# Kernel tuning notes

Hardware: AMD Instinct MI355X
Metric: run time of the kernel (lower is better)

## Reference

```python
import jax, jax.numpy as jnp
import numpy as np

NUM_EXPERTS = 8
DIM = 2048
BATCH = 8192


def setup_inputs() -> dict:
    key = jax.random.key(0)
    k_x, k_ids, k_w, k_b = jax.random.split(key, 4)
    x = jax.random.normal(k_x, (BATCH, DIM), dtype=jnp.float32)
    cam_pred_ids = jax.random.randint(k_ids, (BATCH,), 0, NUM_EXPERTS, dtype=jnp.int64)
    # torch nn.Linear default init: U(-1/sqrt(in), 1/sqrt(in)); W is [out, in]
    bound = 1.0 / np.sqrt(DIM)
    W = jax.random.uniform(k_w, (NUM_EXPERTS, DIM, DIM), dtype=jnp.float32,
                           minval=-bound, maxval=bound)
    b = jax.random.uniform(k_b, (NUM_EXPERTS, DIM), dtype=jnp.float32,
                           minval=-bound, maxval=bound)
    return {"x": x, "cam_pred_ids": cam_pred_ids, "W": W, "b": b}


def reference(x, cam_pred_ids, W, b):
    # Per-sample expert routing: out[i] = x[i] + relu(x[i] @ W[e].T + b[e]),
    # where e = cam_pred_ids[i]. Vectorized as 8 full-batch GEMMs with masked
    # combine (fixed small expert count -> Python loop is structural, not data).
    h = jnp.zeros_like(x)
    for e in range(NUM_EXPERTS):
        he = jax.nn.relu(x @ W[e].T + b[e])          # [B, D]
        mask = (cam_pred_ids == e)[:, None]
        h = h + jnp.where(mask, he, jnp.zeros((), dtype=x.dtype))
    return x + h
```

## Files before the change

### kernel.cpp

```cpp
#include <hip/hip_runtime.h>
#include <hip/hip_bf16.h>
#include <stdint.h>

#define BATCH 8192
#define DIM   2048
#define NEXP  8
#define BM    128
#define BN    128
#define BK    32
#define NITER (DIM / BK)
#define MAX_TILES 72
#define NBLK  (DIM / BN)
#define NCVTB 4096

typedef __bf16 bf16x8 __attribute__((ext_vector_type(8)));
typedef float  f32x4  __attribute__((ext_vector_type(4)));

#define WB_BYTE_OFF 37789696ull
#define WS_NEED     104898560ull

#define AS1(p) ((const __attribute__((address_space(1))) void*)(p))
#define AS3(p) ((__attribute__((address_space(3))) void*)(p))

__device__ __forceinline__ unsigned f2bf2(float lo, float hi) {
    unsigned ul = __float_as_uint(lo), uh = __float_as_uint(hi);
    ul = (ul + 0x7FFFu + ((ul >> 16) & 1u)) >> 16;
    uh = (uh + 0x7FFFu + ((uh >> 16) & 1u)) >> 16;
    return (uh << 16) | ul;
}

__global__ __launch_bounds__(512)
void k_prep(const int* __restrict__ ids, int* __restrict__ ws,
            int* __restrict__ rowmap,
            const float4* __restrict__ W, uint4* __restrict__ Wb) {
    int b = blockIdx.x;
    int t = threadIdx.x;
    if (b > 0) {
        size_t base = (size_t)(b - 1) * 1024;
#pragma unroll
        for (int j = 0; j < 2; j++) {
            size_t o = base + (size_t)j * 512 + t;
            float4 a = W[o * 2], c = W[o * 2 + 1];
            uint4 v;
            v.x = f2bf2(a.x, a.y);  v.y = f2bf2(a.z, a.w);
            v.z = f2bf2(c.x, c.y);  v.w = f2bf2(c.z, c.w);
            Wb[o] = v;
        }
        return;
    }
    __shared__ int sc[512 * NEXP];
    __shared__ int seg[NEXP];
    __shared__ int tot[NEXP];
    int myids[16];
    int base = t * 16;
#pragma unroll
    for (int e = 0; e < NEXP; e++) sc[t * NEXP + e] = 0;
#pragma unroll
    for (int i = 0; i < 16; i++) {
        myids[i] = ids[base + i];
        sc[t * NEXP + myids[i]]++;
    }
    __syncthreads();
    {
        int w = t >> 6, l = t & 63;
        int e = w;
        int vals[8], sum = 0;
#pragma unroll
        for (int j = 0; j < 8; j++) { vals[j] = sc[(l * 8 + j) * NEXP + e]; sum += vals[j]; }
        int inc = sum;
        for (int d = 1; d < 64; d <<= 1) {
            int v = __shfl_up(inc, d, 64);
            if (l >= d) inc += v;
        }
        int run = inc - sum;
#pragma unroll
        for (int j = 0; j < 8; j++) { int v = vals[j]; sc[(l * 8 + j) * NEXP + e] = run; run += v; }
        if (l == 63) tot[e] = run;
    }
    __syncthreads();
    if (t == 0) {
        int pos = 0, mt = 0;
        for (int e = 0; e < NEXP; e++) {
            int c = tot[e];
            seg[e] = pos;
            int ntl = (c + BM - 1) / BM;
            for (int tt = 0; tt < ntl; tt++) {
                ws[64  + mt] = e;
                ws[160 + mt] = pos + tt * BM;
                int v = c - tt * BM;
                ws[256 + mt] = v < BM ? v : BM;
                mt++;
            }
            pos += ntl * BM;
        }
        ws[48] = mt;
    }
    __syncthreads();
#pragma unroll
    for (int i = 0; i < 16; i++) {
        int e = myids[i];
        int p = seg[e] + sc[t * NEXP + e]++;
        rowmap[p] = base + i;
    }
}

__launch_bounds__(256)
__global__ void k_gemm(const float* __restrict__ x,
                       const unsigned short* __restrict__ Wb,
                       const float* __restrict__ bias,
                       const int* __restrict__ ws, const int* __restrict__ rowmap,
                       float* __restrict__ out) {
    int nb = blockIdx.x;
    int mt = blockIdx.y;
    if (mt >= ws[48]) return;
    int e     = ws[64  + mt];
    int pos0  = ws[160 + mt];
    int valid = ws[256 + mt];
    int n0 = nb * BN;

    __shared__ unsigned short lds[2][8192];

    int tid = threadIdx.x;
    int w = tid >> 6, l = tid & 63;
    int lane15 = l & 15, quad = l >> 4;
    int wave_m = (w >> 1) * 64, wave_n = (w & 1) * 64;

    const unsigned short* Bbase = Wb + (size_t)e * DIM * DIM + (size_t)n0 * DIM;

    int arow  = w * 32 + (l >> 1);
    int ahalf = l & 1;
    int s_r = (arow >> 1) & 3;
    int aw0 = arow * BK + (((ahalf * 2)    ) ^ s_r) * 8;
    int aw1 = arow * BK + (((ahalf * 2) + 1) ^ s_r) * 8;
    bool aval = arow < valid;
    const float4* asrc = nullptr;
    if (aval)
        asrc = (const float4*)(x + (size_t)rowmap[pos0 + arow] * DIM + ahalf * 16);

    int srcOff[2];
#pragma unroll
    for (int j = 0; j < 2; j++) {
        int c = w * 128 + j * 64 + l;
        int row = c >> 2, pos = c & 3;
        int q = pos ^ ((row >> 1) & 3);
        srcOff[j] = row * DIM + q * 8;
    }

    int swz = (quad ^ ((lane15 >> 1) & 3)) * 8;
    int afOff[4], bfOff[4];
#pragma unroll
    for (int mi = 0; mi < 4; mi++)
        afOff[mi] = (wave_m + mi * 16 + lane15) * BK + swz;
#pragma unroll
    for (int ni = 0; ni < 4; ni++)
        bfOff[ni] = 4096 + (wave_n + ni * 16 + lane15) * BK + swz;

    f32x4 acc[4][4];
#pragma unroll
    for (int i = 0; i < 4; i++)
#pragma unroll
        for (int j = 0; j < 4; j++) acc[i][j] = (f32x4){0.f, 0.f, 0.f, 0.f};

#define ISSUE_B(buf, k0)                                                        \
    do {                                                                        \
        _Pragma("unroll")                                                       \
        for (int j = 0; j < 2; j++) {                                           \
            __builtin_amdgcn_global_load_lds(                                   \
                AS1(Bbase + (k0) + srcOff[j]),                                  \
                AS3(&lds[buf][4096 + w * 1024 + j * 512]), 16, 0, 0);           \
        }                                                                       \
    } while (0)

#define CVT_WRITE(buf, a0, a1, a2, a3)                                          \
    do {                                                                        \
        bf16x8 c0, c1;                                                          \
        c0[0] = (__bf16)a0.x; c0[1] = (__bf16)a0.y;                             \
        c0[2] = (__bf16)a0.z; c0[3] = (__bf16)a0.w;                             \
        c0[4] = (__bf16)a1.x; c0[5] = (__bf16)a1.y;                             \
        c0[6] = (__bf16)a1.z; c0[7] = (__bf16)a1.w;                             \
        c1[0] = (__bf16)a2.x; c1[1] = (__bf16)a2.y;                             \
        c1[2] = (__bf16)a2.z; c1[3] = (__bf16)a2.w;                             \
        c1[4] = (__bf16)a3.x; c1[5] = (__bf16)a3.y;                             \
        c1[6] = (__bf16)a3.z; c1[7] = (__bf16)a3.w;                             \
        *(bf16x8*)(&lds[buf][aw0]) = c0;                                        \
        *(bf16x8*)(&lds[buf][aw1]) = c1;                                        \
    } while (0)

    {
        float4 a0 = {0,0,0,0}, a1 = {0,0,0,0}, a2 = {0,0,0,0}, a3 = {0,0,0,0};
        if (aval) { a0 = asrc[0]; a1 = asrc[1]; a2 = asrc[2]; a3 = asrc[3]; }
        CVT_WRITE(0, a0, a1, a2, a3);
        ISSUE_B(0, 0);
    }
    int cur = 0;
    for (int i = 0; i < NITER; ++i) {
        __syncthreads();
        float4 a0 = {0,0,0,0}, a1 = {0,0,0,0}, a2 = {0,0,0,0}, a3 = {0,0,0,0};
        if (i + 1 < NITER) {
            if (aval) {
                const float4* p = asrc + (i + 1) * (BK / 4);
                a0 = p[0]; a1 = p[1]; a2 = p[2]; a3 = p[3];
            }
            ISSUE_B(cur ^ 1, (i + 1) * BK);
        }
        bf16x8 af[4], bf[4];
#pragma unroll
        for (int mi = 0; mi < 4; mi++)
            af[mi] = *(const bf16x8*)(&lds[cur][afOff[mi]]);
#pragma unroll
        for (int ni = 0; ni < 4; ni++)
            bf[ni] = *(const bf16x8*)(&lds[cur][bfOff[ni]]);
#pragma unroll
        for (int mi = 0; mi < 4; mi++)
#pragma unroll
            for (int ni = 0; ni < 4; ni++)
                acc[mi][ni] = __builtin_amdgcn_mfma_f32_16x16x32_bf16(
                    af[mi], bf[ni], acc[mi][ni], 0, 0, 0);
        if (i + 1 < NITER)
            CVT_WRITE(cur ^ 1, a0, a1, a2, a3);
        cur ^= 1;
    }
#undef ISSUE_B
#undef CVT_WRITE

    float bv[4];
#pragma unroll
    for (int ni = 0; ni < 4; ni++)
        bv[ni] = bias[(size_t)e * DIM + n0 + wave_n + ni * 16 + lane15];
#pragma unroll
    for (int mi = 0; mi < 4; mi++) {
#pragma unroll
        for (int r4 = 0; r4 < 4; r4++) {
            int rl = wave_m + mi * 16 + quad * 4 + r4;
            if (rl < valid) {
                int orig = rowmap[pos0 + rl];
                const float* xrow = x + (size_t)orig * DIM + n0;
                float* orow = out + (size_t)orig * DIM + n0;
#pragma unroll
                for (int ni = 0; ni < 4; ni++) {
                    int col = wave_n + ni * 16 + lane15;
                    float v = acc[mi][ni][r4] + bv[ni];
                    v = v > 0.f ? v : 0.f;
                    orow[col] = xrow[col] + v;
                }
            }
        }
    }
}

__global__ void k_naive(const float* __restrict__ x, const int* __restrict__ ids,
                        const float* __restrict__ W, const float* __restrict__ b,
                        float* __restrict__ out) {
    __shared__ float lx[DIM];
    int i = blockIdx.x;
    for (int t = threadIdx.x; t < DIM; t += blockDim.x) lx[t] = x[(size_t)i * DIM + t];
    __syncthreads();
    int e = ids[i];
    const float* We = W + (size_t)e * DIM * DIM;
    for (int n = threadIdx.x; n < DIM; n += blockDim.x) {
        const float* wr = We + (size_t)n * DIM;
        float acc = 0.f;
        for (int k = 0; k < DIM; k += 4) {
            float4 w4 = *(const float4*)(wr + k);
            acc += lx[k] * w4.x + lx[k + 1] * w4.y + lx[k + 2] * w4.z + lx[k + 3] * w4.w;
        }
        float v = acc + b[(size_t)e * DIM + n];
        v = v > 0.f ? v : 0.f;
        out[(size_t)i * DIM + n] = lx[n] + v;
    }
}

extern "C" void kernel_launch(void* const* d_in, const int* in_sizes, int n_in,
                              void* d_out, int out_size, void* d_ws, size_t ws_size,
                              hipStream_t stream) {
    const float* x   = (const float*)d_in[0];
    const int*   ids = (const int*)d_in[1];
    const float* W   = (const float*)d_in[2];
    const float* b   = (const float*)d_in[3];
    float* out = (float*)d_out;

    if (ws_size < WS_NEED) {
        k_naive<<<BATCH, 256, 0, stream>>>(x, ids, W, b, out);
        return;
    }

    char* wsb = (char*)d_ws;
    int*  wsi = (int*)wsb;
    unsigned short* Wb = (unsigned short*)(wsb + WB_BYTE_OFF);
    int* rowmap = wsi + 512;

    k_prep<<<NCVTB + 1, 512, 0, stream>>>(ids, wsi, rowmap,
                                          (const float4*)W, (uint4*)Wb);
    dim3 g(NBLK, MAX_TILES);
    k_gemm<<<g, 256, 0, stream>>>(x, Wb, b, wsi, rowmap, out);
}
```

Before: 431.6 us.

## Pre-convert x to bf16 and stream A tiles via direct global-to-LDS loads

```diff
diff --git a/kernel.cpp b/kernel.cpp
--- a/kernel.cpp
+++ b/kernel.cpp
@@ -11,11 +11,15 @@
 #define NITER (DIM / BK)
 #define MAX_TILES 72
 #define NBLK  (DIM / BN)
+#define NROWS 9216
+#define NXBB  2048
 #define NCVTB 4096
 
 typedef __bf16 bf16x8 __attribute__((ext_vector_type(8)));
 typedef float  f32x4  __attribute__((ext_vector_type(4)));
 
+#define ZP_BYTE_OFF 40960ull
+#define XB_BYTE_OFF 49152ull
 #define WB_BYTE_OFF 37789696ull
 #define WS_NEED     104898560ull
 
@@ -32,22 +36,27 @@
 __global__ __launch_bounds__(512)
 void k_prep(const int* __restrict__ ids, int* __restrict__ ws,
             int* __restrict__ rowmap,
-            const float4* __restrict__ W, uint4* __restrict__ Wb) {
+            const float4* __restrict__ x4, uint4* __restrict__ xb4,
+            const float4* __restrict__ W, uint4* __restrict__ Wb,
+            int* __restrict__ zp) {
     int b = blockIdx.x;
     int t = threadIdx.x;
     if (b > 0) {
-        size_t base = (size_t)(b - 1) * 1024;
+        const float4* src; uint4* dst; size_t base;
+        if (b <= NXBB) { src = x4; dst = xb4; base = (size_t)(b - 1) * 1024; }
+        else           { src = W;  dst = Wb;  base = (size_t)(b - 1 - NXBB) * 1024; }
 #pragma unroll
         for (int j = 0; j < 2; j++) {
             size_t o = base + (size_t)j * 512 + t;
-            float4 a = W[o * 2], c = W[o * 2 + 1];
+            float4 a = src[o * 2], c = src[o * 2 + 1];
             uint4 v;
             v.x = f2bf2(a.x, a.y);  v.y = f2bf2(a.z, a.w);
             v.z = f2bf2(c.x, c.y);  v.w = f2bf2(c.z, c.w);
-            Wb[o] = v;
+            dst[o] = v;
         }
         return;
     }
+    zp[t] = 0; zp[t + 512] = 0;
     __shared__ int sc[512 * NEXP];
     __shared__ int seg[NEXP];
     __shared__ int tot[NEXP];
@@ -96,6 +105,8 @@
         ws[48] = mt;
     }
     __syncthreads();
+    for (int i = t; i < NROWS; i += 512) rowmap[i] = -1;
+    __syncthreads();
 #pragma unroll
     for (int i = 0; i < 16; i++) {
         int e = myids[i];
@@ -106,7 +117,9 @@
 
 __launch_bounds__(256)
 __global__ void k_gemm(const float* __restrict__ x,
+                       const unsigned short* __restrict__ xb,
                        const unsigned short* __restrict__ Wb,
+                       const unsigned short* __restrict__ zp,
                        const float* __restrict__ bias,
                        const int* __restrict__ ws, const int* __restrict__ rowmap,
                        float* __restrict__ out) {
@@ -127,23 +140,17 @@
 
     const unsigned short* Bbase = Wb + (size_t)e * DIM * DIM + (size_t)n0 * DIM;
 
-    int arow  = w * 32 + (l >> 1);
-    int ahalf = l & 1;
-    int s_r = (arow >> 1) & 3;
-    int aw0 = arow * BK + (((ahalf * 2)    ) ^ s_r) * 8;
-    int aw1 = arow * BK + (((ahalf * 2) + 1) ^ s_r) * 8;
-    bool aval = arow < valid;
-    const float4* asrc = nullptr;
-    if (aval)
-        asrc = (const float4*)(x + (size_t)rowmap[pos0 + arow] * DIM + ahalf * 16);
-
-    int srcOff[2];
+    const unsigned short* aptr[2];
+    int srcOffB[2];
 #pragma unroll
     for (int j = 0; j < 2; j++) {
         int c = w * 128 + j * 64 + l;
         int row = c >> 2, pos = c & 3;
         int q = pos ^ ((row >> 1) & 3);
-        srcOff[j] = row * DIM + q * 8;
+        int rm = rowmap[pos0 + row];
+        const unsigned short* rb = (rm >= 0) ? (xb + (size_t)rm * DIM) : zp;
+        aptr[j] = rb + q * 8;
+        srcOffB[j] = row * DIM + q * 8;
     }
 
     int swz = (quad ^ ((lane15 >> 1) & 3)) * 8;
@@ -161,47 +168,26 @@
 #pragma unroll
         for (int j = 0; j < 4; j++) acc[i][j] = (f32x4){0.f, 0.f, 0.f, 0.f};
 
-#define ISSUE_B(buf, k0)                                                        \
+#define ISSUE(buf, k0)                                                          \
     do {                                                                        \
         _Pragma("unroll")                                                       \
         for (int j = 0; j < 2; j++) {                                           \
             __builtin_amdgcn_global_load_lds(                                   \
-                AS1(Bbase + (k0) + srcOff[j]),                                  \
+                AS1(aptr[j] + (k0)),                                            \
+                AS3(&lds[buf][w * 1024 + j * 512]), 16, 0, 0);                  \
+            __builtin_amdgcn_global_load_lds(                                   \
+                AS1(Bbase + (k0) + srcOffB[j]),                                 \
                 AS3(&lds[buf][4096 + w * 1024 + j * 512]), 16, 0, 0);           \
         }                                                                       \
     } while (0)
 
-#define CVT_WRITE(buf, a0, a1, a2, a3)                                          \
-    do {                                                                        \
-        bf16x8 c0, c1;                                                          \
-        c0[0] = (__bf16)a0.x; c0[1] = (__bf16)a0.y;                             \
-        c0[2] = (__bf16)a0.z; c0[3] = (__bf16)a0.w;                             \
-        c0[4] = (__bf16)a1.x; c0[5] = (__bf16)a1.y;                             \
-        c0[6] = (__bf16)a1.z; c0[7] = (__bf16)a1.w;                             \
-        c1[0] = (__bf16)a2.x; c1[1] = (__bf16)a2.y;                             \
-        c1[2] = (__bf16)a2.z; c1[3] = (__bf16)a2.w;                             \
-        c1[4] = (__bf16)a3.x; c1[5] = (__bf16)a3.y;                             \
-        c1[6] = (__bf16)a3.z; c1[7] = (__bf16)a3.w;                             \
-        *(bf16x8*)(&lds[buf][aw0]) = c0;                                        \
-        *(bf16x8*)(&lds[buf][aw1]) = c1;                                        \
-    } while (0)
-
-    {
-        float4 a0 = {0,0,0,0}, a1 = {0,0,0,0}, a2 = {0,0,0,0}, a3 = {0,0,0,0};
-        if (aval) { a0 = asrc[0]; a1 = asrc[1]; a2 = asrc[2]; a3 = asrc[3]; }
-        CVT_WRITE(0, a0, a1, a2, a3);
-        ISSUE_B(0, 0);
-    }
+    ISSUE(0, 0);
     int cur = 0;
     for (int i = 0; i < NITER; ++i) {
         __syncthreads();
-        float4 a0 = {0,0,0,0}, a1 = {0,0,0,0}, a2 = {0,0,0,0}, a3 = {0,0,0,0};
         if (i + 1 < NITER) {
-            if (aval) {
-                const float4* p = asrc + (i + 1) * (BK / 4);
-                a0 = p[0]; a1 = p[1]; a2 = p[2]; a3 = p[3];
-            }
-            ISSUE_B(cur ^ 1, (i + 1) * BK);
+            int k0n = (i + 1) * BK;
+            ISSUE(cur ^ 1, k0n);
         }
         bf16x8 af[4], bf[4];
 #pragma unroll
@@ -216,12 +202,9 @@
             for (int ni = 0; ni < 4; ni++)
                 acc[mi][ni] = __builtin_amdgcn_mfma_f32_16x16x32_bf16(
                     af[mi], bf[ni], acc[mi][ni], 0, 0, 0);
-        if (i + 1 < NITER)
-            CVT_WRITE(cur ^ 1, a0, a1, a2, a3);
         cur ^= 1;
     }
-#undef ISSUE_B
-#undef CVT_WRITE
+#undef ISSUE
 
     float bv[4];
 #pragma unroll
@@ -286,11 +269,15 @@
 
     char* wsb = (char*)d_ws;
     int*  wsi = (int*)wsb;
+    int* rowmap = wsi + 512;
+    int* zp = (int*)(wsb + ZP_BYTE_OFF);
+    unsigned short* xb = (unsigned short*)(wsb + XB_BYTE_OFF);
     unsigned short* Wb = (unsigned short*)(wsb + WB_BYTE_OFF);
-    int* rowmap = wsi + 512;
-
-    k_prep<<<NCVTB + 1, 512, 0, stream>>>(ids, wsi, rowmap,
-                                          (const float4*)W, (uint4*)Wb);
+
+    k_prep<<<1 + NXBB + NCVTB, 512, 0, stream>>>(ids, wsi, rowmap,
+                                                 (const float4*)x, (uint4*)xb,
+                                                 (const float4*)W, (uint4*)Wb, zp);
     dim3 g(NBLK, MAX_TILES);
-    k_gemm<<<g, 256, 0, stream>>>(x, Wb, b, wsi, rowmap, out);
-}
+    k_gemm<<<g, 256, 0, stream>>>(x, xb, Wb, (const unsigned short*)zp,
+                                  b, wsi, rowmap, out);
+}
```

After: 407.6 us. -5.6%, faster.
